# Kernel tuning notes

Measured on AMD Instinct MI355X. Metric: run time of the kernel, lower is better.

## Reference

```python
import jax, jax.numpy as jnp
import numpy as np

IN_F = 256
OUT_F = 256
HOP = 3
ALPHA = 0.2   # LeakyReLU negative slope
BETA = 0.5    # hop mixing coefficient
N = 50000
E = 1600000


def setup_inputs() -> dict:
    key = jax.random.key(0)
    k1, k2, k3, k4 = jax.random.split(key, 4)
    inp = jax.random.normal(k1, (N, IN_F), dtype=jnp.float32)
    k_edge_list = jax.random.randint(k2, (HOP, 2, E), 0, N, dtype=jnp.int32)
    # xavier_normal-ish scales
    W = jax.random.normal(k3, (IN_F * HOP, OUT_F), dtype=jnp.float32) * (1.414 * np.sqrt(2.0 / (IN_F * HOP + OUT_F)))
    a = jax.random.normal(k4, (1, 2 * OUT_F * HOP), dtype=jnp.float32) * (1.414 * np.sqrt(2.0 / (1 + 2 * OUT_F * HOP)))
    return {"input": inp, "k_edge_list": k_edge_list, "W": W, "a": a}


def reference(input, k_edge_list, W, a):
    n = input.shape[0]
    h_prime_return = jnp.zeros((n, OUT_F), dtype=input.dtype)
    for i in range(HOP - 1, -1, -1):
        # per-hop projection: h = input @ W[i*in : (i+1)*in]  -> [N, OUT_F]
        h = input @ W[i * IN_F:(i + 1) * IN_F, :]
        src = k_edge_list[i, 0]  # [E] row indices (scatter targets)
        dst = k_edge_list[i, 1]  # [E] col indices (gather sources)
        ai = a[0, 2 * i * OUT_F:(2 * i + 2) * OUT_F]
        # a_i . cat(h[src], h[dst]) == (h @ a_src)[src] + (h @ a_dst)[dst]
        s_src = h @ ai[:OUT_F]   # [N]
        s_dst = h @ ai[OUT_F:]   # [N]
        score = s_src[src] + s_dst[dst]                     # [E]
        edge_e = jnp.exp(-jax.nn.leaky_relu(score, ALPHA))  # [E]
        # sparse row-sum: spmm(A, ones)
        e_rowsum = jax.ops.segment_sum(edge_e, src, num_segments=n)          # [N]
        # weighted aggregate: spmm(A, h)
        h_prime = jax.ops.segment_sum(edge_e[:, None] * h[dst], src, num_segments=n)  # [N, OUT_F]
        h_prime = h_prime / e_rowsum[:, None]
        h_prime_return = (1.0 - BETA) * h_prime + BETA * h_prime_return
    return jax.nn.elu(h_prime_return)  # concat=True path
```

## Files before the change

kernel.cpp:

```cpp
#include <hip/hip_runtime.h>

#define N_NODES 50000
#define E_EDGES 1600000
#define HOPS    3
#define KDIM    256
#define NOUT    768
#define MPAD    50048
#define NPS     50176
#define NCB     196
#define NCB_ALL (NCB * HOPS)
#define HSTRIDE ((size_t)MPAD * 256)
#define FCAP    12288
#define PCAP    10240
#define SEB     4096

typedef unsigned short u16;
typedef __bf16 bf16x8 __attribute__((ext_vector_type(8)));
typedef float  f32x4  __attribute__((ext_vector_type(4)));

__device__ __forceinline__ u16 f2bf(float f) {
  unsigned u = __float_as_uint(f);
  u += 0x7fffu + ((u >> 16) & 1u);
  return (u16)(u >> 16);
}
__device__ __forceinline__ float bf2f(u16 h) {
  return __uint_as_float(((unsigned)h) << 16);
}

__device__ __forceinline__ void gl2lds16(const void* g, void* l) {
  __builtin_amdgcn_global_load_lds(
      (__attribute__((address_space(1))) void*)(g),
      (__attribute__((address_space(3))) void*)(l), 16, 0, 0);
}

__global__ __launch_bounds__(256) void conv_a(const float* __restrict__ in,
                                              u16* __restrict__ A) {
  int idx  = blockIdx.x * 256 + threadIdx.x;
  int base = idx * 4;
  int row  = base >> 8;
  ushort4 o;
  if (row < N_NODES) {
    float4 v = *(const float4*)(in + base);
    o.x = f2bf(v.x); o.y = f2bf(v.y); o.z = f2bf(v.z); o.w = f2bf(v.w);
  } else {
    o.x = 0; o.y = 0; o.z = 0; o.w = 0;
  }
  *(ushort4*)(A + base) = o;
}

__global__ __launch_bounds__(256) void conv_w(const float* __restrict__ W,
                                              u16* __restrict__ Bt) {
  __shared__ float tile[32][33];
  int h  = blockIdx.z;
  int c0 = blockIdx.x * 32;
  int k0 = blockIdx.y * 32;
  int x  = threadIdx.x & 31;
  int y0 = threadIdx.x >> 5;
#pragma unroll
  for (int i = 0; i < 4; ++i) {
    int k = k0 + y0 + i * 8;
    tile[y0 + i * 8][x] = W[(size_t)(h * 256 + k) * 256 + (c0 + x)];
  }
  __syncthreads();
#pragma unroll
  for (int i = 0; i < 4; ++i) {
    int c = c0 + y0 + i * 8;
    Bt[(size_t)(h * 256 + c) * 256 + (k0 + x)] = f2bf(tile[x][y0 + i * 8]);
  }
}

__global__ __launch_bounds__(256) void gemm_kernel(const u16* __restrict__ A,
                                                   const u16* __restrict__ B,
                                                   u16* __restrict__ H,
                                                   const float* __restrict__ a,
                                                   float* __restrict__ ssrc,
                                                   float* __restrict__ sdst) {
  __shared__ char lds[32768];
  int tid  = threadIdx.x;
  int lane = tid & 63;
  int w    = tid >> 6;
  int wm   = w >> 1, wn = w & 1;
  int r    = lane & 15, q = lane >> 4;
  int bm   = blockIdx.y * 128, bn = blockIdx.x * 128;

  const u16* Ag0 = A + (size_t)(bm + 2 * w * 16 + r) * KDIM + q * 8;
  const u16* Bg0 = B + (size_t)(bn + 2 * w * 16 + r) * KDIM + q * 8;

  f32x4 zero = {0.f, 0.f, 0.f, 0.f};
  f32x4 acc[4][4];
#pragma unroll
  for (int mt = 0; mt < 4; ++mt)
#pragma unroll
    for (int nt = 0; nt < 4; ++nt) acc[mt][nt] = zero;

#define STAGE(b, kt)                                                      \
  do {                                                                    \
    int ko = (kt) * 32;                                                   \
    char* As_ = lds + (b) * 16384;                                        \
    char* Bs_ = As_ + 8192;                                               \
    gl2lds16(Ag0 + ko,             As_ + (2 * w) * 1024);                 \
    gl2lds16(Ag0 + 16 * KDIM + ko, As_ + (2 * w + 1) * 1024);             \
    gl2lds16(Bg0 + ko,             Bs_ + (2 * w) * 1024);                 \
    gl2lds16(Bg0 + 16 * KDIM + ko, Bs_ + (2 * w + 1) * 1024);             \
  } while (0)

  STAGE(0, 0);
  __syncthreads();

  for (int kt = 0; kt < 8; ++kt) {
    int cur = kt & 1;
    if (kt < 7) STAGE(cur ^ 1, kt + 1);
    char* As = lds + cur * 16384;
    char* Bs = As + 8192;
    bf16x8 af[4], bfv[4];
#pragma unroll
    for (int mt = 0; mt < 4; ++mt)
      af[mt] = *(const bf16x8*)(As + (wm * 4 + mt) * 1024 + lane * 16);
#pragma unroll
    for (int nt = 0; nt < 4; ++nt)
      bfv[nt] = *(const bf16x8*)(Bs + (wn * 4 + nt) * 1024 + lane * 16);
#pragma unroll
    for (int mt = 0; mt < 4; ++mt)
#pragma unroll
      for (int nt = 0; nt < 4; ++nt)
        acc[mt][nt] = __builtin_amdgcn_mfma_f32_16x16x32_bf16(
            af[mt], bfv[nt], acc[mt][nt], 0, 0, 0);
    if (kt < 7) __syncthreads();
  }
#undef STAGE

  int hop = bn >> 8;
  int cbase = (bn & 255) + wn * 64 + r;
  float asv[4], adv[4];
#pragma unroll
  for (int nt = 0; nt < 4; ++nt) {
    asv[nt] = a[hop * 512 + cbase + nt * 16];
    adv[nt] = a[hop * 512 + 256 + cbase + nt * 16];
  }
#pragma unroll
  for (int mt = 0; mt < 4; ++mt)
#pragma unroll
    for (int rg = 0; rg < 4; ++rg) {
      float ps = 0.f, pd = 0.f;
#pragma unroll
      for (int nt = 0; nt < 4; ++nt) {
        float v = acc[mt][nt][rg];
        ps += v * asv[nt];
        pd += v * adv[nt];
      }
#pragma unroll
      for (int m = 1; m < 16; m <<= 1) {
        ps += __shfl_xor(ps, m);
        pd += __shfl_xor(pd, m);
      }
      if (r == 0) {
        int row = bm + wm * 64 + mt * 16 + q * 4 + rg;
        if (row < N_NODES) {
          atomicAdd(&ssrc[hop * NPS + row], ps);
          atomicAdd(&sdst[hop * NPS + row], pd);
        }
      }
    }

#pragma unroll
  for (int mt = 0; mt < 4; ++mt)
#pragma unroll
    for (int nt = 0; nt < 4; ++nt)
#pragma unroll
      for (int rg = 0; rg < 4; ++rg) {
        int row = bm + wm * 64 + mt * 16 + q * 4 + rg;
        int col = bn + wn * 64 + nt * 16 + r;
        int c = col & 255;
        H[hop * HSTRIDE + (size_t)row * 256 + c] = f2bf(acc[mt][nt][rg]);
      }
}

__global__ __launch_bounds__(256) void init_ccur(int* __restrict__ ccur) {
  int t = blockIdx.x * 256 + threadIdx.x;
  if (t < NCB_ALL) ccur[t] = t * PCAP;
}

__global__ __launch_bounds__(256) void split1_kernel(const int* __restrict__ kel,
                                                     const float* __restrict__ ssrc,
                                                     const float* __restrict__ sdst,
                                                     int* __restrict__ ccur,
                                                     int2* __restrict__ packed) {
  __shared__ int2 stage[SEB];
  __shared__ int h[NCB];
  __shared__ int lofs[NCB];
  __shared__ int bbase[NCB];
  __shared__ int lcur[NCB];
  int t = threadIdx.x, hop = blockIdx.y;
  for (int i = t; i < NCB; i += 256) { h[i] = 0; lcur[i] = 0; }
  __syncthreads();
  const int* srcp = kel + (size_t)hop * 2 * E_EDGES;
  const int* dstp = srcp + E_EDGES;
  int e0 = blockIdx.x * SEB;
  int total = E_EDGES - e0; if (total > SEB) total = SEB;
  int esrc[16], edst[16];
#pragma unroll
  for (int i = 0; i < 16; ++i) {
    int e = e0 + i * 256 + t;
    if (e < E_EDGES) {
      esrc[i] = srcp[e];
      edst[i] = dstp[e];
      atomicAdd(&h[esrc[i] >> 8], 1);
    } else {
      esrc[i] = -1;
    }
  }
  __syncthreads();
  for (int i = t; i < NCB; i += 256)
    if (h[i]) bbase[i] = atomicAdd(&ccur[hop * NCB + i], h[i]);
  if (t < 64) {
    int run = 0;
#pragma unroll
    for (int c = 0; c < 4; ++c) {
      int idx = c * 64 + t;
      int v = (idx < NCB) ? h[idx] : 0;
      int s = v;
#pragma unroll
      for (int d = 1; d < 64; d <<= 1) {
        int x = __shfl_up(s, d);
        if (t >= d) s += x;
      }
      if (idx < NCB) lofs[idx] = run + s - v;
      run += __shfl(s, 63);
    }
  }
  __syncthreads();
#pragma unroll
  for (int i = 0; i < 16; ++i) {
    if (esrc[i] < 0) continue;
    int src = esrc[i], dst = edst[i];
    float s = ssrc[hop * NPS + src] + sdst[hop * NPS + dst];
    float lr = s > 0.0f ? s : 0.2f * s;
    float ee = __expf(-lr);
    int bin = src >> 8;
    int rank = atomicAdd(&lcur[bin], 1);
    stage[lofs[bin] + rank] =
        make_int2((bin << 24) | ((src & 255) << 16) | dst, __float_as_int(ee));
  }
  __syncthreads();
  for (int i = t; i < total; i += 256) {
    int2 r = stage[i];
    int bin = (unsigned)r.x >> 24;
    int pos = bbase[bin] + (i - lofs[bin]);
    packed[pos] = make_int2(r.x & 0x00FFFFFF, r.y);
  }
}

__global__ __launch_bounds__(1024, 1) void fine_kernel(const int* __restrict__ ccur,
                                                       int2* __restrict__ packed,
                                                       int* __restrict__ offs,
                                                       int* __restrict__ counts) {
  __shared__ int2 stage[FCAP];
  __shared__ int h2[256];
  __shared__ int lc[256];
  __shared__ int wtot[4], wbase[4];
  int t = threadIdx.x;
  int b = blockIdx.x;
  int hop = b / NCB, bl = b % NCB;
  int base = b * PCAP;
  int cnt = ccur[b] - base;
  if (cnt > FCAP) cnt = FCAP;
  if (t < 256) h2[t] = 0;
  __syncthreads();
  for (int i = t; i < cnt; i += 1024) {
    int2 r = packed[base + i];
    stage[i] = r;
    atomicAdd(&h2[(r.x >> 16) & 255], 1);
  }
  __syncthreads();
  int v = 0, s = 0;
  if (t < 256) {
    int lane = t & 63;
    v = h2[t];
    s = v;
#pragma unroll
    for (int d = 1; d < 64; d <<= 1) {
      int x = __shfl_up(s, d);
      if (lane >= d) s += x;
    }
    if (lane == 63) wtot[t >> 6] = s;
  }
  __syncthreads();
  if (t == 0) {
    int r = 0;
#pragma unroll
    for (int i = 0; i < 4; ++i) { wbase[i] = r; r += wtot[i]; }
  }
  __syncthreads();
  if (t < 256) {
    int ex = wbase[t >> 6] + s - v;
    int node = hop * NPS + bl * 256 + t;
    offs[node] = base + ex;
    counts[node] = v;
    lc[t] = ex;
  }
  __syncthreads();
  for (int i = t; i < cnt; i += 1024) {
    int2 r = stage[i];
    int low = (r.x >> 16) & 255;
    int rank = atomicAdd(&lc[low], 1);
    packed[base + rank] = make_int2(r.x & 0xFFFF, r.y);
  }
}

__device__ __forceinline__ void accum8(float* a, float& rs, float ee, uint4 h) {
  rs += ee;
  a[0] += ee * __uint_as_float(h.x << 16);
  a[1] += ee * __uint_as_float(h.x & 0xffff0000u);
  a[2] += ee * __uint_as_float(h.y << 16);
  a[3] += ee * __uint_as_float(h.y & 0xffff0000u);
  a[4] += ee * __uint_as_float(h.z << 16);
  a[5] += ee * __uint_as_float(h.z & 0xffff0000u);
  a[6] += ee * __uint_as_float(h.w << 16);
  a[7] += ee * __uint_as_float(h.w & 0xffff0000u);
}

__global__ __launch_bounds__(256) void agg_all(const int* __restrict__ offs,
                                               const int* __restrict__ counts,
                                               const int2* __restrict__ packed,
                                               const u16* __restrict__ Hbf,
                                               float* __restrict__ out) {
  int lane = threadIdx.x & 63, wid = threadIdx.x >> 6;
  int half = lane >> 5, sub = lane & 31;
  int n = blockIdx.x * 4 + wid;
  if (n >= N_NODES) return;

  float r[8];
#pragma unroll
  for (int c = 0; c < 8; ++c) r[c] = 0.f;

#pragma unroll
  for (int hop = 0; hop < HOPS; ++hop) {
    const float wgt = hop == 0 ? 0.5f : (hop == 1 ? 0.25f : 0.125f);
    int start = offs[hop * NPS + n];
    int cnt = counts[hop * NPS + n];
    const int2* pk = packed + start;
    const u16* Hh = Hbf + hop * HSTRIDE + sub * 8;
    float a0[8], a1[8];
    float rs0 = 0.f, rs1 = 0.f;
#pragma unroll
    for (int c = 0; c < 8; ++c) { a0[c] = 0.f; a1[c] = 0.f; }

    int np = cnt >> 1;
    int j = 0;
    for (; j + 8 <= np; j += 8) {
      int2 p[8];
#pragma unroll
      for (int i = 0; i < 8; ++i) p[i] = pk[2 * (j + i) + half];
      uint4 h[8];
#pragma unroll
      for (int i = 0; i < 8; ++i) h[i] = *(const uint4*)(Hh + (size_t)p[i].x * 256);
#pragma unroll
      for (int i = 0; i < 8; ++i)
        accum8((i & 1) ? a1 : a0, (i & 1) ? rs1 : rs0, __int_as_float(p[i].y), h[i]);
    }
    for (; j < np; ++j) {
      int2 p = pk[2 * j + half];
      uint4 hv = *(const uint4*)(Hh + (size_t)p.x * 256);
      accum8(a0, rs0, __int_as_float(p.y), hv);
    }
    if (cnt & 1) {
      int2 p = pk[cnt - 1];
      float ee = half ? 0.f : __int_as_float(p.y);
      uint4 hv = *(const uint4*)(Hh + (size_t)p.x * 256);
      accum8(a1, rs1, ee, hv);
    }

    float rs = rs0 + rs1;
    rs += __shfl_xor(rs, 32);
    float inv = wgt / rs;
#pragma unroll
    for (int c = 0; c < 8; ++c) {
      float t = a0[c] + a1[c];
      t += __shfl_xor(t, 32);
      r[c] += t * inv;
    }
  }

  float* op = out + (size_t)n * 256 + sub * 8 + half * 4;
  float4 o;
  float v0 = r[half * 4 + 0], v1 = r[half * 4 + 1];
  float v2 = r[half * 4 + 2], v3 = r[half * 4 + 3];
  o.x = v0 > 0.f ? v0 : expm1f(v0);
  o.y = v1 > 0.f ? v1 : expm1f(v1);
  o.z = v2 > 0.f ? v2 : expm1f(v2);
  o.w = v3 > 0.f ? v3 : expm1f(v3);
  *(float4*)op = o;
}

extern "C" void kernel_launch(void* const* d_in, const int* in_sizes, int n_in,
                              void* d_out, int out_size, void* d_ws, size_t ws_size,
                              hipStream_t stream) {
  const float* input = (const float*)d_in[0];
  const int*   kel   = (const int*)d_in[1];
  const float* W     = (const float*)d_in[2];
  const float* a     = (const float*)d_in[3];
  float* out = (float*)d_out;

  char* ws = (char*)d_ws;
  size_t o = 0;
  u16* Abf = (u16*)(ws + o);   o += (size_t)MPAD * KDIM * 2;
  u16* Bt  = (u16*)(ws + o);   o += (size_t)NOUT * KDIM * 2;
  u16* Hbf = (u16*)(ws + o);   o += (size_t)MPAD * NOUT * 2;
  float* ssrc = (float*)(ws + o); o += (size_t)3 * NPS * 4;
  float* sdst = (float*)(ws + o); o += (size_t)3 * NPS * 4;
  int* counts = (int*)(ws + o);   o += (size_t)3 * NPS * 4;
  int* offs   = (int*)(ws + o);   o += (size_t)3 * NPS * 4;
  int* ccur   = (int*)(ws + o);   o += 4096;
  int2* packed = (int2*)(ws + o); o += (size_t)NCB_ALL * PCAP * 8 + 65536;

  hipMemsetAsync(ssrc, 0, (size_t)2 * 3 * NPS * 4, stream);

  conv_a<<<MPAD * KDIM / 1024, 256, 0, stream>>>(input, Abf);
  conv_w<<<dim3(8, 8, 3), 256, 0, stream>>>(W, Bt);
  init_ccur<<<3, 256, 0, stream>>>(ccur);
  gemm_kernel<<<dim3(NOUT / 128, MPAD / 128), 256, 0, stream>>>(Abf, Bt, Hbf,
                                                                a, ssrc, sdst);

  int nsplit = (E_EDGES + SEB - 1) / SEB;
  split1_kernel<<<dim3(nsplit, 3), 256, 0, stream>>>(kel, ssrc, sdst, ccur, packed);
  fine_kernel<<<NCB_ALL, 1024, 0, stream>>>(ccur, packed, offs, counts);

  agg_all<<<N_NODES / 4 + 1, 256, 0, stream>>>(offs, counts, packed, Hbf, out);
}
```

Measured before the change: 640.0 us.

## Keep fine-sort records in registers instead of LDS and split aggregation launches

The fine bucket-sort kernel drops its 96KB LDS staging array and holds up to nine records per thread in registers, re-reading them for the scatter pass. This frees LDS and removes the one-block-per-CU launch bound, so more fine blocks can be resident at once. The per-bucket cap falls from 12288 to 9216 edges, which could truncate heavier buckets. Aggregation is also split into five launches over node ranges, which adds launch overhead and may be aimed at cache locality.

```diff
diff --git a/kernel.cpp b/kernel.cpp
--- a/kernel.cpp
+++ b/kernel.cpp
@@ -10,8 +10,8 @@
 #define NCB     196
 #define NCB_ALL (NCB * HOPS)
 #define HSTRIDE ((size_t)MPAD * 256)
-#define FCAP    12288
 #define PCAP    10240
+#define RCAP    9216
 #define SEB     4096
 
 typedef unsigned short u16;
@@ -250,11 +250,10 @@
   }
 }
 
-__global__ __launch_bounds__(1024, 1) void fine_kernel(const int* __restrict__ ccur,
-                                                       int2* __restrict__ packed,
-                                                       int* __restrict__ offs,
-                                                       int* __restrict__ counts) {
-  __shared__ int2 stage[FCAP];
+__global__ __launch_bounds__(1024) void fine_kernel(const int* __restrict__ ccur,
+                                                    int2* __restrict__ packed,
+                                                    int* __restrict__ offs,
+                                                    int* __restrict__ counts) {
   __shared__ int h2[256];
   __shared__ int lc[256];
   __shared__ int wtot[4], wbase[4];
@@ -263,14 +262,21 @@
   int hop = b / NCB, bl = b % NCB;
   int base = b * PCAP;
   int cnt = ccur[b] - base;
-  if (cnt > FCAP) cnt = FCAP;
+  if (cnt > RCAP) cnt = RCAP;
   if (t < 256) h2[t] = 0;
   __syncthreads();
-  for (int i = t; i < cnt; i += 1024) {
-    int2 r = packed[base + i];
-    stage[i] = r;
-    atomicAdd(&h2[(r.x >> 16) & 255], 1);
-  }
+  int2 r0, r1, r2, r3, r4, r5, r6, r7, r8;
+#define FLOAD(k, rv)                                                     \
+  do {                                                                   \
+    int idx = (k) * 1024 + t;                                            \
+    if (idx < cnt) {                                                     \
+      rv = packed[base + idx];                                           \
+      atomicAdd(&h2[(rv.x >> 16) & 255], 1);                             \
+    }                                                                    \
+  } while (0)
+  FLOAD(0, r0); FLOAD(1, r1); FLOAD(2, r2); FLOAD(3, r3); FLOAD(4, r4);
+  FLOAD(5, r5); FLOAD(6, r6); FLOAD(7, r7); FLOAD(8, r8);
+#undef FLOAD
   __syncthreads();
   int v = 0, s = 0;
   if (t < 256) {
@@ -299,12 +305,18 @@
     lc[t] = ex;
   }
   __syncthreads();
-  for (int i = t; i < cnt; i += 1024) {
-    int2 r = stage[i];
-    int low = (r.x >> 16) & 255;
-    int rank = atomicAdd(&lc[low], 1);
-    packed[base + rank] = make_int2(r.x & 0xFFFF, r.y);
-  }
+#define FSCAT(k, rv)                                                     \
+  do {                                                                   \
+    int idx = (k) * 1024 + t;                                            \
+    if (idx < cnt) {                                                     \
+      int low = (rv.x >> 16) & 255;                                      \
+      int rank = atomicAdd(&lc[low], 1);                                 \
+      packed[base + rank] = make_int2(rv.x & 0xFFFF, rv.y);              \
+    }                                                                    \
+  } while (0)
+  FSCAT(0, r0); FSCAT(1, r1); FSCAT(2, r2); FSCAT(3, r3); FSCAT(4, r4);
+  FSCAT(5, r5); FSCAT(6, r6); FSCAT(7, r7); FSCAT(8, r8);
+#undef FSCAT
 }
 
 __device__ __forceinline__ void accum8(float* a, float& rs, float ee, uint4 h) {
@@ -323,11 +335,12 @@
                                                const int* __restrict__ counts,
                                                const int2* __restrict__ packed,
                                                const u16* __restrict__ Hbf,
-                                               float* __restrict__ out) {
+                                               float* __restrict__ out,
+                                               int n0, int n1) {
   int lane = threadIdx.x & 63, wid = threadIdx.x >> 6;
   int half = lane >> 5, sub = lane & 31;
-  int n = blockIdx.x * 4 + wid;
-  if (n >= N_NODES) return;
+  int n = n0 + blockIdx.x * 4 + wid;
+  if (n >= n1) return;
 
   float r[8];
 #pragma unroll
@@ -425,5 +438,9 @@
   split1_kernel<<<dim3(nsplit, 3), 256, 0, stream>>>(kel, ssrc, sdst, ccur, packed);
   fine_kernel<<<NCB_ALL, 1024, 0, stream>>>(ccur, packed, offs, counts);
 
-  agg_all<<<N_NODES / 4 + 1, 256, 0, stream>>>(offs, counts, packed, Hbf, out);
-}
+  agg_all<<<2500, 256, 0, stream>>>(offs, counts, packed, Hbf, out, 0, 10000);
+  agg_all<<<2500, 256, 0, stream>>>(offs, counts, packed, Hbf, out, 10000, 20000);
+  agg_all<<<2500, 256, 0, stream>>>(offs, counts, packed, Hbf, out, 20000, 30000);
+  agg_all<<<2500, 256, 0, stream>>>(offs, counts, packed, Hbf, out, 30000, 40000);
+  agg_all<<<2500, 256, 0, stream>>>(offs, counts, packed, Hbf, out, 40000, 50000);
+}
```

Result: slower. 671.5 us (+4.9%).
